# Kernel tuning notes

Measured on AMD Instinct MI355X. Metric: run time of the kernel, lower is better.

## Reference

```python
import jax, jax.numpy as jnp
import numpy as np

EPS = 1e-5

def ter_quant(w):
    # BitNet b1.58 absmean ternary quantization: scale by mean(|W|), round to {-1,0,1}, rescale.
    gamma = jnp.mean(jnp.abs(w)) + EPS
    wq = jnp.clip(jnp.round(w / gamma), -1.0, 1.0) * gamma
    return wq

def setup_inputs() -> dict:
    key = jax.random.key(0)
    k_x, k_w1, k_w2 = jax.random.split(key, 3)
    B, S, D, H = 64, 197, 768, 3072
    x = jax.random.normal(k_x, (B, S, D), dtype=jnp.float32)
    w1 = jax.random.normal(k_w1, (H, D), dtype=jnp.float32) * (1.0 / np.sqrt(D))
    b1 = jnp.zeros((H,), dtype=jnp.float32)
    w2 = jax.random.normal(k_w2, (D, H), dtype=jnp.float32) * (1.0 / np.sqrt(H))
    b2 = jnp.zeros((D,), dtype=jnp.float32)
    return {"x": x, "w1": w1, "b1": b1, "w2": w2, "b2": b2}

def reference(x, w1, b1, w2, b2):
    # fc1: ternary-quantized linear, exact GELU, fc2: ternary-quantized linear (dropout p=0 is identity)
    h = jnp.einsum('bsd,hd->bsh', x, ter_quant(w1)) + b1
    h = jax.nn.gelu(h, approximate=False)
    y = jnp.einsum('bsh,dh->bsd', h, ter_quant(w2)) + b2
    return y
```

## Files before the change

kernel.cpp:

```cpp
#include <hip/hip_runtime.h>
#include <hip/hip_bf16.h>
#include <math.h>

typedef __bf16 bf16_t;
typedef __bf16 bf16x8 __attribute__((ext_vector_type(8)));
typedef float f32x4 __attribute__((ext_vector_type(4)));

#define QEPS 1e-5

__device__ __forceinline__ void gload_lds16(const void* g, void* l) {
  __builtin_amdgcn_global_load_lds((const __attribute__((address_space(1))) void*)g,
                                   (__attribute__((address_space(3))) void*)l, 16, 0, 0);
}

__device__ __forceinline__ float gelu_exact(float x) {
  float a = x * 0.7071067811865476f;
  float s = fabsf(a);
  float t = __builtin_amdgcn_rcpf(__builtin_fmaf(0.3275911f, s, 1.0f));
  float p = __builtin_fmaf(1.061405429f, t, -1.453152027f);
  p = __builtin_fmaf(p, t, 1.421413741f);
  p = __builtin_fmaf(p, t, -0.284496736f);
  p = __builtin_fmaf(p, t, 0.254829592f);
  p = p * t;
  float e = __expf(-s * s);
  float er = copysignf(__builtin_fmaf(-p, e, 1.0f), a);
  return 0.5f * x * (1.0f + er);
}

__global__ void reduce_part_kernel(const float* __restrict__ w1, const float* __restrict__ w2,
                                   int n, double* __restrict__ part) {
  const bool second = blockIdx.x >= 256;
  const float* __restrict__ w = second ? w2 : w1;
  const int b = second ? blockIdx.x - 256 : blockIdx.x;
  double s = 0.0;
  const int stride = 256 * 256 * 4;
  for (int i = (b * 256 + threadIdx.x) * 4; i < n; i += stride) {
    float4 v = *(const float4*)(w + i);
    s += (double)fabsf(v.x) + (double)fabsf(v.y) + (double)fabsf(v.z) + (double)fabsf(v.w);
  }
  for (int off = 32; off > 0; off >>= 1)
    s += __shfl_down(s, off, 64);
  __shared__ double ls[4];
  int lane = threadIdx.x & 63, wv = threadIdx.x >> 6;
  if (lane == 0) ls[wv] = s;
  __syncthreads();
  if (threadIdx.x == 0) part[blockIdx.x] = ls[0] + ls[1] + ls[2] + ls[3];
}

__global__ void prep_kernel(const float* __restrict__ w1, const float* __restrict__ w2,
                            const float* __restrict__ x, const double* __restrict__ part,
                            double* __restrict__ gammas, bf16_t* __restrict__ q1,
                            bf16_t* __restrict__ q2, bf16_t* __restrict__ xb) {
  const int tid = threadIdx.x;
  const int b = blockIdx.x;
  if (b < 2304) {
    const bool second = b >= 1152;
    double p = part[(second ? 256 : 0) + tid];
    for (int off = 32; off > 0; off >>= 1)
      p += __shfl_down(p, off, 64);
    __shared__ double red[4];
    if ((tid & 63) == 0) red[tid >> 6] = p;
    __syncthreads();
    const double g = (red[0] + red[1] + red[2] + red[3]) / 2359296.0 + QEPS;
    if (tid == 0 && (b == 0 || b == 1152)) gammas[second ? 1 : 0] = g;
    const double rg = 1.0 / g;
    const int gchunk = (second ? b - 1152 : b) * 256 + tid;
    const int tile = gchunk >> 9, cidx = gchunk & 511;
    const int r = cidx >> 2, slot = cidx & 3, cch = slot ^ (r & 3);
    int row, colbase, C;
    if (second) { C = 3072; row = (tile / 96) * 128 + r; colbase = (tile % 96) * 32 + cch * 8; }
    else        { C = 768;  row = (tile / 24) * 128 + r; colbase = (tile % 24) * 32 + cch * 8; }
    const float* __restrict__ W = second ? w2 : w1;
    const float4 v0 = *(const float4*)(W + (size_t)row * C + colbase);
    const float4 v1 = *(const float4*)(W + (size_t)row * C + colbase + 4);
    bf16x8 o;
    o[0] = (bf16_t)(float)fmin(1.0, fmax(-1.0, rint((double)v0.x * rg)));
    o[1] = (bf16_t)(float)fmin(1.0, fmax(-1.0, rint((double)v0.y * rg)));
    o[2] = (bf16_t)(float)fmin(1.0, fmax(-1.0, rint((double)v0.z * rg)));
    o[3] = (bf16_t)(float)fmin(1.0, fmax(-1.0, rint((double)v0.w * rg)));
    o[4] = (bf16_t)(float)fmin(1.0, fmax(-1.0, rint((double)v1.x * rg)));
    o[5] = (bf16_t)(float)fmin(1.0, fmax(-1.0, rint((double)v1.y * rg)));
    o[6] = (bf16_t)(float)fmin(1.0, fmax(-1.0, rint((double)v1.z * rg)));
    o[7] = (bf16_t)(float)fmin(1.0, fmax(-1.0, rint((double)v1.w * rg)));
    *(bf16x8*)((second ? q2 : q1) + (size_t)gchunk * 8) = o;
  } else {
    const int gchunk = (b - 2304) * 256 + tid;
    const int tile = gchunk >> 9, cidx = gchunk & 511;
    const int r = cidx >> 2, slot = cidx & 3, cch = slot ^ (r & 3);
    const int row = (tile / 24) * 128 + r;
    const int colbase = (tile % 24) * 32 + cch * 8;
    bf16x8 o;
    if (row < 12608) {
      const float4 v0 = *(const float4*)(x + (size_t)row * 768 + colbase);
      const float4 v1 = *(const float4*)(x + (size_t)row * 768 + colbase + 4);
      o[0] = (bf16_t)v0.x; o[1] = (bf16_t)v0.y; o[2] = (bf16_t)v0.z; o[3] = (bf16_t)v0.w;
      o[4] = (bf16_t)v1.x; o[5] = (bf16_t)v1.y; o[6] = (bf16_t)v1.z; o[7] = (bf16_t)v1.w;
    } else {
      o = bf16x8{};
    }
    *(bf16x8*)(xb + (size_t)gchunk * 8) = o;
  }
}

template <int EPI, int NJ>
__global__ __launch_bounds__(256, (NJ == 8 ? 2 : 3))
void gemm_tiled(const bf16_t* __restrict__ A, const bf16_t* __restrict__ B,
                const float* __restrict__ bias, const double* __restrict__ gptr,
                void* __restrict__ Cout, int nkt, int gx, int Mvalid, int aux) {
  constexpr int BN = NJ * 32;
  constexpr int BTILE = BN * 32;
  constexpr int NRTB = BN / 128;
  __shared__ bf16_t sm[2 * 4096 + 2 * BTILE];
  bf16_t* const sA0 = sm;
  bf16_t* const sB0 = sm + 2 * 4096;

  const int G = gridDim.x;
  const int f = blockIdx.x;
  const int xcd = f & 7;
  const int idx = f >> 3;
  const int q8 = G >> 3, r8 = G & 7;
  const int t = xcd * q8 + (xcd < r8 ? xcd : r8) + idx;
  const int bx = t % gx;
  const int by = t / gx;

  const int tid = threadIdx.x;
  const int lane = tid & 63;
  const int wave = tid >> 6;
  const int wr = (wave >> 1) * 64;
  const int wc = (wave & 1) * (BN / 2);
  const int row16 = lane & 15;
  const int quad = lane >> 4;

  const bf16_t* gA = A + ((size_t)by * nkt) * 4096 + tid * 8;
  const bf16_t* gB0 = B + ((size_t)(bx * NRTB) * nkt) * 4096 + tid * 8;
  const bf16_t* gB1 = (NJ == 8) ? B + ((size_t)(bx * NRTB + 1) * nkt) * 4096 + tid * 8 : nullptr;
  const int lws = wave * 512;

  f32x4 acc[4][NJ] = {};

  {
    gload_lds16(gA, sA0 + lws);
    gload_lds16(gA + 2048, sA0 + 2048 + lws);
    gload_lds16(gB0, sB0 + lws);
    gload_lds16(gB0 + 2048, sB0 + 2048 + lws);
    if constexpr (NJ == 8) {
      gload_lds16(gB1, sB0 + 4096 + lws);
      gload_lds16(gB1 + 2048, sB0 + 6144 + lws);
    }
    gA += 4096; gB0 += 4096;
    if constexpr (NJ == 8) gB1 += 4096;
  }
  __syncthreads();

  int p = 0;
  const int sw = (quad ^ (row16 & 3)) * 8;
  for (int kt = 0; kt < nkt; kt++) {
    if (kt + 1 < nkt) {
      bf16_t* dA = sA0 + (p ^ 1) * 4096;
      bf16_t* dB = sB0 + (p ^ 1) * BTILE;
      gload_lds16(gA, dA + lws);
      gload_lds16(gA + 2048, dA + 2048 + lws);
      gload_lds16(gB0, dB + lws);
      gload_lds16(gB0 + 2048, dB + 2048 + lws);
      if constexpr (NJ == 8) {
        gload_lds16(gB1, dB + 4096 + lws);
        gload_lds16(gB1 + 2048, dB + 6144 + lws);
      }
      gA += 4096; gB0 += 4096;
      if constexpr (NJ == 8) gB1 += 4096;
    }
    const bf16_t* sA = sA0 + p * 4096;
    const bf16_t* sB = sB0 + p * BTILE;
    bf16x8 afr[4], bfr[NJ];
#pragma unroll
    for (int i = 0; i < 4; i++)
      afr[i] = *(const bf16x8*)&sA[(wr + i * 16 + row16) * 32 + sw];
#pragma unroll
    for (int j = 0; j < NJ; j++)
      bfr[j] = *(const bf16x8*)&sB[(wc + j * 16 + row16) * 32 + sw];
#pragma unroll
    for (int i = 0; i < 4; i++)
#pragma unroll
      for (int j = 0; j < NJ; j++)
        acc[i][j] = __builtin_amdgcn_mfma_f32_16x16x32_bf16(afr[i], bfr[j], acc[i][j], 0, 0, 0);
    __syncthreads();
    p ^= 1;
  }

  const float gamma = (float)gptr[0];

  if constexpr (EPI == 0) {
    constexpr int SEW = BN + 8;
    bf16_t* sE = sm;
    bf16_t* h = (bf16_t*)Cout;
    float bv[NJ];
#pragma unroll
    for (int j = 0; j < NJ; j++) bv[j] = bias[bx * BN + wc + row16 + j * 16];
    const int ktBase = bx * (BN / 32);
#pragma unroll
    for (int i = 0; i < 4; i++) {
#pragma unroll
      for (int j = 0; j < NJ; j++) {
        const int col = wc + j * 16 + row16;
#pragma unroll
        for (int r = 0; r < 4; r++) {
          const int e = (wave >> 1) * 16 + quad * 4 + r;
          sE[e * SEW + col] = (bf16_t)gelu_exact(gamma * acc[i][j][r] + bv[j]);
        }
      }
      __syncthreads();
      {
        const int e2 = tid >> 3, chb = tid & 7;
        const int r_in = (e2 >> 4) * 64 + i * 16 + (e2 & 15);
#pragma unroll
        for (int cc = 0; cc < BN / 64; cc++) {
          const int c = chb + cc * 8;
          const int kt_o = ktBase + (c >> 2);
          const int slot = (c & 3) ^ (r_in & 3);
          const size_t off = ((size_t)(by * aux + kt_o)) * 4096 + r_in * 32 + slot * 8;
          *(bf16x8*)&h[off] = *(const bf16x8*)&sE[e2 * SEW + c * 8];
        }
      }
      __syncthreads();
    }
  } else {
    float* out = (float*)Cout;
    const int c_base = bx * BN + wc + row16;
    const int r_base = by * 128 + wr + quad * 4;
#pragma unroll
    for (int j = 0; j < NJ; j++) {
      const int col = c_base + j * 16;
      const float bv = bias[col];
#pragma unroll
      for (int i = 0; i < 4; i++) {
#pragma unroll
        for (int r = 0; r < 4; r++) {
          const int row = r_base + i * 16 + r;
          if (row < Mvalid)
            out[(size_t)row * aux + col] = gamma * acc[i][j][r] + bv;
        }
      }
    }
  }
}

extern "C" void kernel_launch(void* const* d_in, const int* in_sizes, int n_in,
                              void* d_out, int out_size, void* d_ws, size_t ws_size,
                              hipStream_t stream) {
  const float* x  = (const float*)d_in[0];
  const float* w1 = (const float*)d_in[1];
  const float* b1 = (const float*)d_in[2];
  const float* w2 = (const float*)d_in[3];
  const float* b2 = (const float*)d_in[4];
  float* out = (float*)d_out;

  const int M = 64 * 197;
  const int Mpad = 12672;
  const int D = 768, H = 3072;
  const int nW = H * D;

  char* ws = (char*)d_ws;
  double* part = (double*)ws;
  double* gammas = (double*)(ws + 4096);
  bf16_t* xb  = (bf16_t*)(ws + 4096 + 256);
  bf16_t* w1q = xb + (size_t)Mpad * D;
  bf16_t* w2q = w1q + (size_t)H * D;
  bf16_t* hb  = w2q + (size_t)D * H;

  reduce_part_kernel<<<512, 256, 0, stream>>>(w1, w2, nW, part);
  prep_kernel<<<2304 + 4752, 256, 0, stream>>>(w1, w2, x, part, gammas, w1q, w2q, xb);

  gemm_tiled<0, 8><<<99 * 12, 256, 0, stream>>>(xb, w1q, b1, gammas + 0, hb, 24, 12, M, H / 32);
  gemm_tiled<1, 4><<<99 * 6, 256, 0, stream>>>(hb, w2q, b2, gammas + 1, out, 96, 6, M, D);
}
```

Measured before the change: 250.6 us.

## Replace GEMM with 256x256 tile, 8-wave kernel and 64-wide K tiles

Replaces the 128xBN, 4-wave GEMM with a 512-thread kernel that computes 256x256 output tiles with a 64-element K step. It uses 128KB of dynamic LDS and a staged schedule that interleaves async global-to-LDS loads with four MFMA quadrants under s_setprio, separated by barriers. The prep kernel and the GELU epilogue are changed to the new 128x64 swizzled tile layout, and M is padded to 12800. The aim is more data reuse per byte loaded and better overlap of loads with MFMA. The cost is lower occupancy, many more barriers, and a small grid for fc2 (150 blocks) that may not fill the GPU.

```diff
diff --git a/kernel.cpp b/kernel.cpp
--- a/kernel.cpp
+++ b/kernel.cpp
@@ -65,14 +65,14 @@
     if (tid == 0 && (b == 0 || b == 1152)) gammas[second ? 1 : 0] = g;
     const double rg = 1.0 / g;
     const int gchunk = (second ? b - 1152 : b) * 256 + tid;
-    const int tile = gchunk >> 9, cidx = gchunk & 511;
-    const int r = cidx >> 2, slot = cidx & 3, cch = slot ^ (r & 3);
-    int row, colbase, C;
-    if (second) { C = 3072; row = (tile / 96) * 128 + r; colbase = (tile % 96) * 32 + cch * 8; }
-    else        { C = 768;  row = (tile / 24) * 128 + r; colbase = (tile % 24) * 32 + cch * 8; }
-    const float* __restrict__ W = second ? w2 : w1;
-    const float4 v0 = *(const float4*)(W + (size_t)row * C + colbase);
-    const float4 v1 = *(const float4*)(W + (size_t)row * C + colbase + 4);
+    const int tile = gchunk >> 10, cidx = gchunk & 1023;
+    const int r = cidx >> 3, slot = cidx & 7, kc = slot ^ (r & 7);
+    int row, col, C;
+    const float* __restrict__ W;
+    if (second) { C = 3072; W = w2; row = (tile / 48) * 128 + r; col = (tile % 48) * 64 + kc * 8; }
+    else        { C = 768;  W = w1; row = (tile / 12) * 128 + r; col = (tile % 12) * 64 + kc * 8; }
+    const float4 v0 = *(const float4*)(W + (size_t)row * C + col);
+    const float4 v1 = *(const float4*)(W + (size_t)row * C + col + 4);
     bf16x8 o;
     o[0] = (bf16_t)(float)fmin(1.0, fmax(-1.0, rint((double)v0.x * rg)));
     o[1] = (bf16_t)(float)fmin(1.0, fmax(-1.0, rint((double)v0.y * rg)));
@@ -85,14 +85,14 @@
     *(bf16x8*)((second ? q2 : q1) + (size_t)gchunk * 8) = o;
   } else {
     const int gchunk = (b - 2304) * 256 + tid;
-    const int tile = gchunk >> 9, cidx = gchunk & 511;
-    const int r = cidx >> 2, slot = cidx & 3, cch = slot ^ (r & 3);
-    const int row = (tile / 24) * 128 + r;
-    const int colbase = (tile % 24) * 32 + cch * 8;
+    const int tile = gchunk >> 10, cidx = gchunk & 1023;
+    const int r = cidx >> 3, slot = cidx & 7, kc = slot ^ (r & 7);
+    const int row = (tile / 12) * 128 + r;
+    const int col = (tile % 12) * 64 + kc * 8;
     bf16x8 o;
     if (row < 12608) {
-      const float4 v0 = *(const float4*)(x + (size_t)row * 768 + colbase);
-      const float4 v1 = *(const float4*)(x + (size_t)row * 768 + colbase + 4);
+      const float4 v0 = *(const float4*)(x + (size_t)row * 768 + col);
+      const float4 v1 = *(const float4*)(x + (size_t)row * 768 + col + 4);
       o[0] = (bf16_t)v0.x; o[1] = (bf16_t)v0.y; o[2] = (bf16_t)v0.z; o[3] = (bf16_t)v0.w;
       o[4] = (bf16_t)v1.x; o[5] = (bf16_t)v1.y; o[6] = (bf16_t)v1.z; o[7] = (bf16_t)v1.w;
     } else {
@@ -102,17 +102,12 @@
   }
 }
 
-template <int EPI, int NJ>
-__global__ __launch_bounds__(256, (NJ == 8 ? 2 : 3))
-void gemm_tiled(const bf16_t* __restrict__ A, const bf16_t* __restrict__ B,
-                const float* __restrict__ bias, const double* __restrict__ gptr,
-                void* __restrict__ Cout, int nkt, int gx, int Mvalid, int aux) {
-  constexpr int BN = NJ * 32;
-  constexpr int BTILE = BN * 32;
-  constexpr int NRTB = BN / 128;
-  __shared__ bf16_t sm[2 * 4096 + 2 * BTILE];
-  bf16_t* const sA0 = sm;
-  bf16_t* const sB0 = sm + 2 * 4096;
+template <int EPI>
+__global__ __launch_bounds__(512, 2)
+void gemm8(const bf16_t* __restrict__ A, const bf16_t* __restrict__ B,
+           const float* __restrict__ bias, const double* __restrict__ gptr,
+           void* __restrict__ Cout, int nkt, int gx, int Mvalid, int aux) {
+  extern __shared__ bf16_t smem[];
 
   const int G = gridDim.x;
   const int f = blockIdx.x;
@@ -126,122 +121,149 @@
   const int tid = threadIdx.x;
   const int lane = tid & 63;
   const int wave = tid >> 6;
-  const int wr = (wave >> 1) * 64;
-  const int wc = (wave & 1) * (BN / 2);
   const int row16 = lane & 15;
   const int quad = lane >> 4;
-
-  const bf16_t* gA = A + ((size_t)by * nkt) * 4096 + tid * 8;
-  const bf16_t* gB0 = B + ((size_t)(bx * NRTB) * nkt) * 4096 + tid * 8;
-  const bf16_t* gB1 = (NJ == 8) ? B + ((size_t)(bx * NRTB + 1) * nkt) * 4096 + tid * 8 : nullptr;
-  const int lws = wave * 512;
-
-  f32x4 acc[4][NJ] = {};
-
-  {
-    gload_lds16(gA, sA0 + lws);
-    gload_lds16(gA + 2048, sA0 + 2048 + lws);
-    gload_lds16(gB0, sB0 + lws);
-    gload_lds16(gB0 + 2048, sB0 + 2048 + lws);
-    if constexpr (NJ == 8) {
-      gload_lds16(gB1, sB0 + 4096 + lws);
-      gload_lds16(gB1 + 2048, sB0 + 6144 + lws);
-    }
-    gA += 4096; gB0 += 4096;
-    if constexpr (NJ == 8) gB1 += 4096;
-  }
-  __syncthreads();
-
-  int p = 0;
-  const int sw = (quad ^ (row16 & 3)) * 8;
-  for (int kt = 0; kt < nkt; kt++) {
-    if (kt + 1 < nkt) {
-      bf16_t* dA = sA0 + (p ^ 1) * 4096;
-      bf16_t* dB = sB0 + (p ^ 1) * BTILE;
-      gload_lds16(gA, dA + lws);
-      gload_lds16(gA + 2048, dA + 2048 + lws);
-      gload_lds16(gB0, dB + lws);
-      gload_lds16(gB0 + 2048, dB + 2048 + lws);
-      if constexpr (NJ == 8) {
-        gload_lds16(gB1, dB + 4096 + lws);
-        gload_lds16(gB1 + 2048, dB + 6144 + lws);
-      }
-      gA += 4096; gB0 += 4096;
-      if constexpr (NJ == 8) gB1 += 4096;
-    }
-    const bf16_t* sA = sA0 + p * 4096;
-    const bf16_t* sB = sB0 + p * BTILE;
-    bf16x8 afr[4], bfr[NJ];
-#pragma unroll
-    for (int i = 0; i < 4; i++)
-      afr[i] = *(const bf16x8*)&sA[(wr + i * 16 + row16) * 32 + sw];
-#pragma unroll
-    for (int j = 0; j < NJ; j++)
-      bfr[j] = *(const bf16x8*)&sB[(wc + j * 16 + row16) * 32 + sw];
-#pragma unroll
-    for (int i = 0; i < 4; i++)
-#pragma unroll
-      for (int j = 0; j < NJ; j++)
-        acc[i][j] = __builtin_amdgcn_mfma_f32_16x16x32_bf16(afr[i], bfr[j], acc[i][j], 0, 0, 0);
-    __syncthreads();
-    p ^= 1;
+  const int ww = wave >> 2;
+  const int wcol = wave & 3;
+
+  const int sw0 = (quad ^ (row16 & 7)) * 8;
+  const int aoff0 = row16 * 64 + sw0;
+  const int aoff1 = row16 * 64 + (sw0 ^ 32);
+  const int wwoff = ww * 4096;
+  const int bcoff = wcol * 2048;
+
+  const bf16_t* const Ab = A + (size_t)(by * 2) * nkt * 8192;
+  const bf16_t* const Bb = B + (size_t)(bx * 2) * nkt * 8192;
+
+  f32x4 acc[8][4] = {};
+  bf16x8 aw[8], bw0[4], bw1[4];
+
+#define SA_(bufv, h) (smem + (((bufv) * 2 + (h)) * 8192))
+#define SB_(bufv, h) (smem + 32768 + (((bufv) * 2 + (h)) * 8192))
+#define SRCA_(T, h) (Ab + ((size_t)(h) * nkt + (T)) * 8192)
+#define SRCB_(T, h) (Bb + ((size_t)(h) * nkt + (T)) * 8192)
+#define STAGE_(src, dst) do { \
+    gload_lds16((src) + tid * 8, (dst) + wave * 512); \
+    gload_lds16((src) + 4096 + tid * 8, (dst) + 4096 + wave * 512); } while (0)
+#define LDA_(bufv, h) do { \
+    const bf16_t* p0_ = SA_(bufv, h) + wwoff + aoff0; \
+    const bf16_t* p1_ = SA_(bufv, h) + wwoff + aoff1; \
+    aw[0] = *(const bf16x8*)(p0_);        aw[1] = *(const bf16x8*)(p1_); \
+    aw[2] = *(const bf16x8*)(p0_ + 1024); aw[3] = *(const bf16x8*)(p1_ + 1024); \
+    aw[4] = *(const bf16x8*)(p0_ + 2048); aw[5] = *(const bf16x8*)(p1_ + 2048); \
+    aw[6] = *(const bf16x8*)(p0_ + 3072); aw[7] = *(const bf16x8*)(p1_ + 3072); } while (0)
+#define LDB_(arr, bufv, h) do { \
+    const bf16_t* p0_ = SB_(bufv, h) + bcoff + aoff0; \
+    const bf16_t* p1_ = SB_(bufv, h) + bcoff + aoff1; \
+    arr[0] = *(const bf16x8*)(p0_);        arr[1] = *(const bf16x8*)(p1_); \
+    arr[2] = *(const bf16x8*)(p0_ + 1024); arr[3] = *(const bf16x8*)(p1_ + 1024); } while (0)
+#define MMQ_(BW, AM0, AN0) do { \
+    __builtin_amdgcn_s_setprio(1); \
+    _Pragma("unroll") for (int m_ = 0; m_ < 4; m_++) \
+    _Pragma("unroll") for (int n_ = 0; n_ < 2; n_++) \
+    _Pragma("unroll") for (int k_ = 0; k_ < 2; k_++) \
+      acc[(AM0) + m_][(AN0) + n_] = __builtin_amdgcn_mfma_f32_16x16x32_bf16( \
+          aw[2 * m_ + k_], BW[2 * n_ + k_], acc[(AM0) + m_][(AN0) + n_], 0, 0, 0); \
+    __builtin_amdgcn_s_setprio(0); } while (0)
+
+  STAGE_(SRCA_(0, 0), SA_(0, 0));
+  STAGE_(SRCB_(0, 0), SB_(0, 0));
+  STAGE_(SRCB_(0, 1), SB_(0, 1));
+  STAGE_(SRCA_(0, 1), SA_(0, 1));
+  STAGE_(SRCA_(1, 0), SA_(1, 0));
+  STAGE_(SRCB_(1, 0), SB_(1, 0));
+  asm volatile("s_waitcnt vmcnt(4)" ::: "memory");
+  __builtin_amdgcn_s_barrier();
+
+  for (int T = 0; T < nkt; T++) {
+    const int buf = T & 1;
+    LDA_(buf, 0);
+    LDB_(bw0, buf, 0);
+    if (T + 1 < nkt) STAGE_(SRCB_(T + 1, 1), SB_(buf ^ 1, 1));
+    __builtin_amdgcn_s_barrier();
+    MMQ_(bw0, 0, 0);
+    __builtin_amdgcn_s_barrier();
+    LDB_(bw1, buf, 1);
+    if (T + 1 < nkt) STAGE_(SRCA_(T + 1, 1), SA_(buf ^ 1, 1));
+    __builtin_amdgcn_s_barrier();
+    MMQ_(bw1, 0, 2);
+    __builtin_amdgcn_s_barrier();
+    LDA_(buf, 1);
+    if (T + 2 < nkt) STAGE_(SRCA_(T + 2, 0), SA_(buf, 0));
+    __builtin_amdgcn_s_barrier();
+    MMQ_(bw0, 4, 0);
+    __builtin_amdgcn_s_barrier();
+    if (T + 2 < nkt) STAGE_(SRCB_(T + 2, 0), SB_(buf, 0));
+    __builtin_amdgcn_s_barrier();
+    MMQ_(bw1, 4, 2);
+    if (T + 2 < nkt) asm volatile("s_waitcnt vmcnt(4)" ::: "memory");
+    else             asm volatile("s_waitcnt vmcnt(0)" ::: "memory");
+    __builtin_amdgcn_s_barrier();
   }
 
   const float gamma = (float)gptr[0];
 
+  float bv[4];
+  int cbv[4];
+#pragma unroll
+  for (int an = 0; an < 4; an++) {
+    cbv[an] = (an >> 1) * 128 + wcol * 32 + (an & 1) * 16 + row16;
+    bv[an] = bias[bx * 256 + cbv[an]];
+  }
+
   if constexpr (EPI == 0) {
-    constexpr int SEW = BN + 8;
-    bf16_t* sE = sm;
-    bf16_t* h = (bf16_t*)Cout;
-    float bv[NJ];
-#pragma unroll
-    for (int j = 0; j < NJ; j++) bv[j] = bias[bx * BN + wc + row16 + j * 16];
-    const int ktBase = bx * (BN / 32);
-#pragma unroll
-    for (int i = 0; i < 4; i++) {
-#pragma unroll
-      for (int j = 0; j < NJ; j++) {
-        const int col = wc + j * 16 + row16;
+    bf16_t* sE = smem;
+#pragma unroll
+    for (int am = 0; am < 8; am++) {
+      const int rtile = am >> 2;
+      const int rbase = ww * 64 + (am & 3) * 16 + quad * 4;
+#pragma unroll
+      for (int an = 0; an < 4; an++) {
+        const int cb = cbv[an];
+        const int ltile = rtile * 4 + (cb >> 6);
+        const int kc = (cb >> 3) & 7, e = cb & 7;
 #pragma unroll
         for (int r = 0; r < 4; r++) {
-          const int e = (wave >> 1) * 16 + quad * 4 + r;
-          sE[e * SEW + col] = (bf16_t)gelu_exact(gamma * acc[i][j][r] + bv[j]);
-        }
-      }
-      __syncthreads();
-      {
-        const int e2 = tid >> 3, chb = tid & 7;
-        const int r_in = (e2 >> 4) * 64 + i * 16 + (e2 & 15);
-#pragma unroll
-        for (int cc = 0; cc < BN / 64; cc++) {
-          const int c = chb + cc * 8;
-          const int kt_o = ktBase + (c >> 2);
-          const int slot = (c & 3) ^ (r_in & 3);
-          const size_t off = ((size_t)(by * aux + kt_o)) * 4096 + r_in * 32 + slot * 8;
-          *(bf16x8*)&h[off] = *(const bf16x8*)&sE[e2 * SEW + c * 8];
-        }
-      }
-      __syncthreads();
-    }
-  } else {
-    float* out = (float*)Cout;
-    const int c_base = bx * BN + wc + row16;
-    const int r_base = by * 128 + wr + quad * 4;
-#pragma unroll
-    for (int j = 0; j < NJ; j++) {
-      const int col = c_base + j * 16;
-      const float bv = bias[col];
-#pragma unroll
-      for (int i = 0; i < 4; i++) {
-#pragma unroll
-        for (int r = 0; r < 4; r++) {
-          const int row = r_base + i * 16 + r;
-          if (row < Mvalid)
-            out[(size_t)row * aux + col] = gamma * acc[i][j][r] + bv;
+          const int rin = rbase + r;
+          sE[ltile * 8192 + (rin * 8 + (kc ^ (rin & 7))) * 8 + e] =
+              (bf16_t)gelu_exact(__builtin_fmaf(gamma, acc[am][an][r], bv[an]));
         }
       }
     }
-  }
+    __syncthreads();
+    bf16_t* hb = (bf16_t*)Cout;
+#pragma unroll
+    for (int i = 0; i < 16; i++) {
+      const int gc = i * 512 + tid;
+      const int lt = gc >> 10, ci = gc & 1023;
+      const int rg = by * 2 + (lt >> 2), kg = bx * 4 + (lt & 3);
+      *(bf16x8*)(hb + ((size_t)rg * aux + kg) * 8192 + ci * 8) = *(const bf16x8*)(sE + gc * 8);
+    }
+  } else {
+    float* outp = (float*)Cout;
+#pragma unroll
+    for (int am = 0; am < 8; am++) {
+      const int rbase = by * 256 + (am >> 2) * 128 + ww * 64 + (am & 3) * 16 + quad * 4;
+#pragma unroll
+      for (int an = 0; an < 4; an++) {
+        const int col = bx * 256 + cbv[an];
+#pragma unroll
+        for (int r = 0; r < 4; r++) {
+          const int row = rbase + r;
+          if (row < Mvalid)
+            outp[(size_t)row * aux + col] = __builtin_fmaf(gamma, acc[am][an][r], bv[an]);
+        }
+      }
+    }
+  }
+#undef SA_
+#undef SB_
+#undef SRCA_
+#undef SRCB_
+#undef STAGE_
+#undef LDA_
+#undef LDB_
+#undef MMQ_
 }
 
 extern "C" void kernel_launch(void* const* d_in, const int* in_sizes, int n_in,
@@ -255,7 +277,7 @@
   float* out = (float*)d_out;
 
   const int M = 64 * 197;
-  const int Mpad = 12672;
+  const int Mpad = 12800;
   const int D = 768, H = 3072;
   const int nW = H * D;
 
@@ -267,9 +289,18 @@
   bf16_t* w2q = w1q + (size_t)H * D;
   bf16_t* hb  = w2q + (size_t)D * H;
 
+  static bool attr_done = false;
+  if (!attr_done) {
+    (void)hipFuncSetAttribute(reinterpret_cast<const void*>(&gemm8<0>),
+                              hipFuncAttributeMaxDynamicSharedMemorySize, 131072);
+    (void)hipFuncSetAttribute(reinterpret_cast<const void*>(&gemm8<1>),
+                              hipFuncAttributeMaxDynamicSharedMemorySize, 131072);
+    attr_done = true;
+  }
+
   reduce_part_kernel<<<512, 256, 0, stream>>>(w1, w2, nW, part);
-  prep_kernel<<<2304 + 4752, 256, 0, stream>>>(w1, w2, x, part, gammas, w1q, w2q, xb);
-
-  gemm_tiled<0, 8><<<99 * 12, 256, 0, stream>>>(xb, w1q, b1, gammas + 0, hb, 24, 12, M, H / 32);
-  gemm_tiled<1, 4><<<99 * 6, 256, 0, stream>>>(hb, w2q, b2, gammas + 1, out, 96, 6, M, D);
-}
+  prep_kernel<<<2304 + 4800, 256, 0, stream>>>(w1, w2, x, part, gammas, w1q, w2q, xb);
+
+  gemm8<0><<<50 * 12, 512, 131072, stream>>>(xb, w1q, b1, gammas + 0, hb, 12, 12, M, H / 64);
+  gemm8<1><<<50 * 3, 512, 131072, stream>>>(hb, w2q, b2, gammas + 1, out, 48, 3, M, D);
+}
```

Measured after the change: 300.5 us. 19.9% more time.

## Switch GEMMs to 128x128 tiles with 64-wide K steps and 8-way swizzle

Applied to the files above, without the earlier changes.

The packed bf16 tile layout produced by the prep kernel changes from 32-wide K chunks with a 4-slot XOR swizzle to 64-wide K chunks with an 8-slot swizzle. Both GEMMs become a single 128x128-tile kernel using 64 KB of dynamic LDS. Each K step now issues two MFMAs per fragment, which halves the number of K iterations and barriers. The fc1 GELU epilogue now writes the whole tile to LDS once before copying it out, and Mpad is raised to 12800 to fit 100 row tiles. The fc1 tile shrinks from 128x256 to 128x128, which lowers reuse per block and doubles the grid, while the larger LDS footprint may limit occupancy.

```diff
diff --git a/kernel.cpp b/kernel.cpp
--- a/kernel.cpp
+++ b/kernel.cpp
@@ -65,14 +65,14 @@
     if (tid == 0 && (b == 0 || b == 1152)) gammas[second ? 1 : 0] = g;
     const double rg = 1.0 / g;
     const int gchunk = (second ? b - 1152 : b) * 256 + tid;
-    const int tile = gchunk >> 9, cidx = gchunk & 511;
-    const int r = cidx >> 2, slot = cidx & 3, cch = slot ^ (r & 3);
-    int row, colbase, C;
-    if (second) { C = 3072; row = (tile / 96) * 128 + r; colbase = (tile % 96) * 32 + cch * 8; }
-    else        { C = 768;  row = (tile / 24) * 128 + r; colbase = (tile % 24) * 32 + cch * 8; }
-    const float* __restrict__ W = second ? w2 : w1;
-    const float4 v0 = *(const float4*)(W + (size_t)row * C + colbase);
-    const float4 v1 = *(const float4*)(W + (size_t)row * C + colbase + 4);
+    const int tile = gchunk >> 10, cidx = gchunk & 1023;
+    const int r = cidx >> 3, slot = cidx & 7, kc = slot ^ (r & 7);
+    int row, col, C;
+    const float* __restrict__ W;
+    if (second) { C = 3072; W = w2; row = (tile / 48) * 128 + r; col = (tile % 48) * 64 + kc * 8; }
+    else        { C = 768;  W = w1; row = (tile / 12) * 128 + r; col = (tile % 12) * 64 + kc * 8; }
+    const float4 v0 = *(const float4*)(W + (size_t)row * C + col);
+    const float4 v1 = *(const float4*)(W + (size_t)row * C + col + 4);
     bf16x8 o;
     o[0] = (bf16_t)(float)fmin(1.0, fmax(-1.0, rint((double)v0.x * rg)));
     o[1] = (bf16_t)(float)fmin(1.0, fmax(-1.0, rint((double)v0.y * rg)));
@@ -85,14 +85,14 @@
     *(bf16x8*)((second ? q2 : q1) + (size_t)gchunk * 8) = o;
   } else {
     const int gchunk = (b - 2304) * 256 + tid;
-    const int tile = gchunk >> 9, cidx = gchunk & 511;
-    const int r = cidx >> 2, slot = cidx & 3, cch = slot ^ (r & 3);
-    const int row = (tile / 24) * 128 + r;
-    const int colbase = (tile % 24) * 32 + cch * 8;
+    const int tile = gchunk >> 10, cidx = gchunk & 1023;
+    const int r = cidx >> 3, slot = cidx & 7, kc = slot ^ (r & 7);
+    const int row = (tile / 12) * 128 + r;
+    const int col = (tile % 12) * 64 + kc * 8;
     bf16x8 o;
     if (row < 12608) {
-      const float4 v0 = *(const float4*)(x + (size_t)row * 768 + colbase);
-      const float4 v1 = *(const float4*)(x + (size_t)row * 768 + colbase + 4);
+      const float4 v0 = *(const float4*)(x + (size_t)row * 768 + col);
+      const float4 v1 = *(const float4*)(x + (size_t)row * 768 + col + 4);
       o[0] = (bf16_t)v0.x; o[1] = (bf16_t)v0.y; o[2] = (bf16_t)v0.z; o[3] = (bf16_t)v0.w;
       o[4] = (bf16_t)v1.x; o[5] = (bf16_t)v1.y; o[6] = (bf16_t)v1.z; o[7] = (bf16_t)v1.w;
     } else {
@@ -102,17 +102,12 @@
   }
 }
 
-template <int EPI, int NJ>
-__global__ __launch_bounds__(256, (NJ == 8 ? 2 : 3))
-void gemm_tiled(const bf16_t* __restrict__ A, const bf16_t* __restrict__ B,
-                const float* __restrict__ bias, const double* __restrict__ gptr,
-                void* __restrict__ Cout, int nkt, int gx, int Mvalid, int aux) {
-  constexpr int BN = NJ * 32;
-  constexpr int BTILE = BN * 32;
-  constexpr int NRTB = BN / 128;
-  __shared__ bf16_t sm[2 * 4096 + 2 * BTILE];
-  bf16_t* const sA0 = sm;
-  bf16_t* const sB0 = sm + 2 * 4096;
+template <int EPI>
+__global__ __launch_bounds__(256, 2)
+void gemm_db(const bf16_t* __restrict__ A, const bf16_t* __restrict__ B,
+             const float* __restrict__ bias, const double* __restrict__ gptr,
+             void* __restrict__ Cout, int nkt, int gx, int Mvalid, int aux) {
+  extern __shared__ bf16_t sm[];
 
   const int G = gridDim.x;
   const int f = blockIdx.x;
@@ -126,119 +121,111 @@
   const int tid = threadIdx.x;
   const int lane = tid & 63;
   const int wave = tid >> 6;
-  const int wr = (wave >> 1) * 64;
-  const int wc = (wave & 1) * (BN / 2);
   const int row16 = lane & 15;
   const int quad = lane >> 4;
-
-  const bf16_t* gA = A + ((size_t)by * nkt) * 4096 + tid * 8;
-  const bf16_t* gB0 = B + ((size_t)(bx * NRTB) * nkt) * 4096 + tid * 8;
-  const bf16_t* gB1 = (NJ == 8) ? B + ((size_t)(bx * NRTB + 1) * nkt) * 4096 + tid * 8 : nullptr;
-  const int lws = wave * 512;
-
-  f32x4 acc[4][NJ] = {};
-
-  {
-    gload_lds16(gA, sA0 + lws);
-    gload_lds16(gA + 2048, sA0 + 2048 + lws);
-    gload_lds16(gB0, sB0 + lws);
-    gload_lds16(gB0 + 2048, sB0 + 2048 + lws);
-    if constexpr (NJ == 8) {
-      gload_lds16(gB1, sB0 + 4096 + lws);
-      gload_lds16(gB1 + 2048, sB0 + 6144 + lws);
-    }
-    gA += 4096; gB0 += 4096;
-    if constexpr (NJ == 8) gB1 += 4096;
+  const int wr = (wave >> 1) * 64;
+  const int wc = (wave & 1) * 64;
+  const int sw0 = (quad ^ (row16 & 7)) * 8;
+  const int sw1 = sw0 ^ 32;
+
+  const bf16_t* const gA = A + (size_t)by * nkt * 8192;
+  const bf16_t* const gB = B + (size_t)bx * nkt * 8192;
+
+  f32x4 acc[4][4] = {};
+
+  const int o8 = tid * 8;
+  const int w512 = wave * 512;
+
+#pragma unroll
+  for (int l = 0; l < 4; l++) {
+    gload_lds16(gA + l * 2048 + o8, sm + l * 2048 + w512);
+    gload_lds16(gB + l * 2048 + o8, sm + 16384 + l * 2048 + w512);
   }
   __syncthreads();
 
   int p = 0;
-  const int sw = (quad ^ (row16 & 3)) * 8;
-  for (int kt = 0; kt < nkt; kt++) {
-    if (kt + 1 < nkt) {
-      bf16_t* dA = sA0 + (p ^ 1) * 4096;
-      bf16_t* dB = sB0 + (p ^ 1) * BTILE;
-      gload_lds16(gA, dA + lws);
-      gload_lds16(gA + 2048, dA + 2048 + lws);
-      gload_lds16(gB0, dB + lws);
-      gload_lds16(gB0 + 2048, dB + 2048 + lws);
-      if constexpr (NJ == 8) {
-        gload_lds16(gB1, dB + 4096 + lws);
-        gload_lds16(gB1 + 2048, dB + 6144 + lws);
-      }
-      gA += 4096; gB0 += 4096;
-      if constexpr (NJ == 8) gB1 += 4096;
-    }
-    const bf16_t* sA = sA0 + p * 4096;
-    const bf16_t* sB = sB0 + p * BTILE;
-    bf16x8 afr[4], bfr[NJ];
+  for (int T = 0; T < nkt; T++) {
+    if (T + 1 < nkt) {
+      const bf16_t* sa = gA + (size_t)(T + 1) * 8192;
+      const bf16_t* sb = gB + (size_t)(T + 1) * 8192;
+      bf16_t* dA = sm + (p ^ 1) * 8192;
+      bf16_t* dB = sm + 16384 + (p ^ 1) * 8192;
+#pragma unroll
+      for (int l = 0; l < 4; l++) {
+        gload_lds16(sa + l * 2048 + o8, dA + l * 2048 + w512);
+        gload_lds16(sb + l * 2048 + o8, dB + l * 2048 + w512);
+      }
+    }
+    const bf16_t* sA = sm + p * 8192;
+    const bf16_t* sB = sm + 16384 + p * 8192;
+    bf16x8 aw[4][2], bw[4][2];
+#pragma unroll
+    for (int i = 0; i < 4; i++) {
+      const bf16_t* pr = sA + (wr + i * 16 + row16) * 64;
+      aw[i][0] = *(const bf16x8*)(pr + sw0);
+      aw[i][1] = *(const bf16x8*)(pr + sw1);
+    }
+#pragma unroll
+    for (int j = 0; j < 4; j++) {
+      const bf16_t* pr = sB + (wc + j * 16 + row16) * 64;
+      bw[j][0] = *(const bf16x8*)(pr + sw0);
+      bw[j][1] = *(const bf16x8*)(pr + sw1);
+    }
 #pragma unroll
     for (int i = 0; i < 4; i++)
-      afr[i] = *(const bf16x8*)&sA[(wr + i * 16 + row16) * 32 + sw];
-#pragma unroll
-    for (int j = 0; j < NJ; j++)
-      bfr[j] = *(const bf16x8*)&sB[(wc + j * 16 + row16) * 32 + sw];
-#pragma unroll
-    for (int i = 0; i < 4; i++)
-#pragma unroll
-      for (int j = 0; j < NJ; j++)
-        acc[i][j] = __builtin_amdgcn_mfma_f32_16x16x32_bf16(afr[i], bfr[j], acc[i][j], 0, 0, 0);
+#pragma unroll
+      for (int j = 0; j < 4; j++) {
+        acc[i][j] = __builtin_amdgcn_mfma_f32_16x16x32_bf16(aw[i][0], bw[j][0], acc[i][j], 0, 0, 0);
+        acc[i][j] = __builtin_amdgcn_mfma_f32_16x16x32_bf16(aw[i][1], bw[j][1], acc[i][j], 0, 0, 0);
+      }
     __syncthreads();
     p ^= 1;
   }
 
   const float gamma = (float)gptr[0];
+  float bv[4];
+#pragma unroll
+  for (int j = 0; j < 4; j++) bv[j] = bias[bx * 128 + wc + j * 16 + row16];
 
   if constexpr (EPI == 0) {
-    constexpr int SEW = BN + 8;
+    constexpr int SEW = 136;
     bf16_t* sE = sm;
-    bf16_t* h = (bf16_t*)Cout;
-    float bv[NJ];
-#pragma unroll
-    for (int j = 0; j < NJ; j++) bv[j] = bias[bx * BN + wc + row16 + j * 16];
-    const int ktBase = bx * (BN / 32);
 #pragma unroll
     for (int i = 0; i < 4; i++) {
-#pragma unroll
-      for (int j = 0; j < NJ; j++) {
+      const int rb = wr + i * 16 + quad * 4;
+#pragma unroll
+      for (int j = 0; j < 4; j++) {
         const int col = wc + j * 16 + row16;
 #pragma unroll
-        for (int r = 0; r < 4; r++) {
-          const int e = (wave >> 1) * 16 + quad * 4 + r;
-          sE[e * SEW + col] = (bf16_t)gelu_exact(gamma * acc[i][j][r] + bv[j]);
-        }
-      }
-      __syncthreads();
-      {
-        const int e2 = tid >> 3, chb = tid & 7;
-        const int r_in = (e2 >> 4) * 64 + i * 16 + (e2 & 15);
-#pragma unroll
-        for (int cc = 0; cc < BN / 64; cc++) {
-          const int c = chb + cc * 8;
-          const int kt_o = ktBase + (c >> 2);
-          const int slot = (c & 3) ^ (r_in & 3);
-          const size_t off = ((size_t)(by * aux + kt_o)) * 4096 + r_in * 32 + slot * 8;
-          *(bf16x8*)&h[off] = *(const bf16x8*)&sE[e2 * SEW + c * 8];
-        }
-      }
-      __syncthreads();
+        for (int r = 0; r < 4; r++)
+          sE[(rb + r) * SEW + col] =
+              (bf16_t)gelu_exact(__builtin_fmaf(gamma, acc[i][j][r], bv[j]));
+      }
+    }
+    __syncthreads();
+    bf16_t* hb = (bf16_t*)Cout;
+#pragma unroll
+    for (int kh = 0; kh < 2; kh++) {
+      bf16_t* ht = hb + ((size_t)by * aux + bx * 2 + kh) * 8192;
+#pragma unroll
+      for (int n = 0; n < 4; n++) {
+        const int g = n * 256 + tid;
+        const int r = g >> 3, slot = g & 7, c = slot ^ (r & 7);
+        *(bf16x8*)(ht + g * 8) = *(const bf16x8*)(sE + r * SEW + kh * 64 + c * 8);
+      }
     }
   } else {
-    float* out = (float*)Cout;
-    const int c_base = bx * BN + wc + row16;
-    const int r_base = by * 128 + wr + quad * 4;
-#pragma unroll
-    for (int j = 0; j < NJ; j++) {
-      const int col = c_base + j * 16;
-      const float bv = bias[col];
+    float* outp = (float*)Cout;
+#pragma unroll
+    for (int j = 0; j < 4; j++) {
+      const int col = bx * 128 + wc + j * 16 + row16;
 #pragma unroll
       for (int i = 0; i < 4; i++) {
-#pragma unroll
-        for (int r = 0; r < 4; r++) {
-          const int row = r_base + i * 16 + r;
-          if (row < Mvalid)
-            out[(size_t)row * aux + col] = gamma * acc[i][j][r] + bv;
-        }
+        const int rb = by * 128 + wr + i * 16 + quad * 4;
+#pragma unroll
+        for (int r = 0; r < 4; r++)
+          if (rb + r < Mvalid)
+            outp[(size_t)(rb + r) * aux + col] = __builtin_fmaf(gamma, acc[i][j][r], bv[j]);
       }
     }
   }
@@ -255,7 +242,7 @@
   float* out = (float*)d_out;
 
   const int M = 64 * 197;
-  const int Mpad = 12672;
+  const int Mpad = 12800;
   const int D = 768, H = 3072;
   const int nW = H * D;
 
@@ -267,9 +254,18 @@
   bf16_t* w2q = w1q + (size_t)H * D;
   bf16_t* hb  = w2q + (size_t)D * H;
 
+  static bool attr_done = false;
+  if (!attr_done) {
+    (void)hipFuncSetAttribute(reinterpret_cast<const void*>(&gemm_db<0>),
+                              hipFuncAttributeMaxDynamicSharedMemorySize, 65536);
+    (void)hipFuncSetAttribute(reinterpret_cast<const void*>(&gemm_db<1>),
+                              hipFuncAttributeMaxDynamicSharedMemorySize, 65536);
+    attr_done = true;
+  }
+
   reduce_part_kernel<<<512, 256, 0, stream>>>(w1, w2, nW, part);
-  prep_kernel<<<2304 + 4752, 256, 0, stream>>>(w1, w2, x, part, gammas, w1q, w2q, xb);
-
-  gemm_tiled<0, 8><<<99 * 12, 256, 0, stream>>>(xb, w1q, b1, gammas + 0, hb, 24, 12, M, H / 32);
-  gemm_tiled<1, 4><<<99 * 6, 256, 0, stream>>>(hb, w2q, b2, gammas + 1, out, 96, 6, M, D);
-}
+  prep_kernel<<<2304 + 4800, 256, 0, stream>>>(w1, w2, x, part, gammas, w1q, w2q, xb);
+
+  gemm_db<0><<<100 * 24, 256, 65536, stream>>>(xb, w1q, b1, gammas + 0, hb, 12, 24, M, H / 64);
+  gemm_db<1><<<100 * 6, 256, 65536, stream>>>(hb, w2q, b2, gammas + 1, out, 48, 6, M, D);
+}
```

Result: slower. 275.0 us (+9.7%).
